# Kernel tuning notes

Hardware: AMD Instinct MI355X
Metric: run time of the kernel (lower is better)

## Reference

```python
import jax, jax.numpy as jnp
import numpy as np
from jax.scipy.special import logsumexp

S, D, K, R, P = 500, 768, 16, 256, 64  # seq_len, bert_dim, out_dim, n_pairs, max wordpieces/entity


def setup_inputs() -> dict:
    key = jax.random.key(0)
    k1, k2, k3, k4, k5, k6 = jax.random.split(key, 6)
    word_embeddings = jax.random.normal(k1, (S, D), jnp.float32)
    # kaiming_normal_ fan_in = D*K (last two dims collapsed); gain sqrt(2) for relu
    W = jax.random.normal(k2, (D, K, D), jnp.float32) * np.float32((2.0 / (K * D)) ** 0.5)
    idx1 = jax.random.randint(k3, (R, P), 0, S)
    idx2 = jax.random.randint(k4, (R, P), 0, S)
    # ragged mention lengths -> padding masks (at least 1 valid wordpiece)
    len1 = jax.random.randint(k5, (R,), 1, P + 1)
    len2 = jax.random.randint(k6, (R,), 1, P + 1)
    pos = jnp.arange(P)
    mask1 = (pos[None, :] < len1[:, None]).astype(jnp.float32)
    mask2 = (pos[None, :] < len2[:, None]).astype(jnp.float32)
    return {"word_embeddings": word_embeddings, "W": W, "idx1": idx1, "idx2": idx2,
            "mask1": mask1, "mask2": mask2}


def reference(word_embeddings, W, idx1, idx2, mask1, mask2):
    # gather ragged mention wordpieces (padded to P per entity)
    e1 = word_embeddings[idx1]  # [R, P, D]
    e2 = word_embeddings[idx2]  # [R, P, D]
    # biaffine: z[r,k,p,q] = e1[r,p,:] @ W[:,k,:] @ e2[r,q,:]
    zh = jnp.einsum('rpd,dke->rpke', e1, W)      # [R, P, K, D]
    z = jnp.einsum('rpke,rqe->rkpq', zh, e2)     # [R, K, P, P]
    # logsumexp pooling over all valid (p, q) mention-token pairs
    b = mask1[:, None, :, None] * mask2[:, None, None, :]  # [R, 1, P, P]
    scores = logsumexp(z, axis=(2, 3), b=b)      # [R, K]
    return scores
```

## Files before the change

### kernel.cpp

```cpp
#include <hip/hip_runtime.h>
#include <math.h>

#define S_ 500
#define D_ 768
#define K_ 16
#define R_ 256
#define P_ 64
#define NT 12

typedef unsigned short ushort_t;
typedef __attribute__((ext_vector_type(8))) short short8;
typedef __attribute__((ext_vector_type(4))) float floatx4;

__device__ inline ushort_t f2bf(float x) {
  unsigned int u = __float_as_uint(x);
  u += 0x7fffu + ((u >> 16) & 1u);
  return (ushort_t)(u >> 16);
}

#define GLD_LDS16(g, l)                                                        \
  __builtin_amdgcn_global_load_lds(                                            \
      (const __attribute__((address_space(1))) void*)(g),                      \
      (__attribute__((address_space(3))) void*)(l), 16, 0, 0)

#define ASM_BARRIER asm volatile("s_barrier" ::: "memory")
#define WAIT_VM8 asm volatile("s_waitcnt vmcnt(8)" ::: "memory")
#define WAIT_VM6 asm volatile("s_waitcnt vmcnt(6)" ::: "memory")
#define WAIT_VM0 asm volatile("s_waitcnt vmcnt(0)" ::: "memory")

__global__ __launch_bounds__(256) void prep(const float* __restrict__ WE,
                                            const float* __restrict__ W,
                                            ushort_t* __restrict__ WEb,
                                            ushort_t* __restrict__ Wt) {
  const int t = threadIdx.x;
  if (blockIdx.x < 384) {
    int gid = blockIdx.x * 256 + t;
    int row = gid / 192;
    ushort4 o = {0, 0, 0, 0};
    if (row < S_) {
      float4 v = *(const float4*)(WE + (size_t)gid * 4);
      o.x = f2bf(v.x); o.y = f2bf(v.y); o.z = f2bf(v.z); o.w = f2bf(v.w);
    }
    *(ushort4*)(WEb + (size_t)gid * 4) = o;
    return;
  }
  __shared__ float tile[64][68];
  const int tb = blockIdx.x - 384;
  const int n0 = (tb % 192) * 64, d0 = (tb / 192) * 64;
  {
    const int r = t >> 2, cbase = (t & 3) * 16;
#pragma unroll
    for (int i = 0; i < 4; i++) {
      float4 v = *(const float4*)(W + (size_t)(d0 + r) * 12288 + n0 + cbase + i * 4);
      *(float4*)&tile[r][cbase + i * 4] = v;
    }
  }
  __syncthreads();
  {
    const int bc = t & 15;
    const int br4 = (t >> 4) * 4;
    float4 tv[4];
#pragma unroll
    for (int ii = 0; ii < 4; ii++)
      tv[ii] = *(const float4*)&tile[bc * 4 + ii][br4];
#pragma unroll
    for (int j = 0; j < 4; j++) {
      ushort4 o;
      o.x = f2bf(((const float*)&tv[0])[j]);
      o.y = f2bf(((const float*)&tv[1])[j]);
      o.z = f2bf(((const float*)&tv[2])[j]);
      o.w = f2bf(((const float*)&tv[3])[j]);
      *(ushort4*)(Wt + (size_t)(n0 + br4 + j) * 768 + d0 + bc * 4) = o;
    }
  }
}

__global__ __launch_bounds__(256, 2) void mm0_bt(const ushort_t* __restrict__ A,
                                                 const ushort_t* __restrict__ Bm,
                                                 ushort_t* __restrict__ C) {
  __shared__ ushort_t As[2][2][128 * 32];
  __shared__ ushort_t Bs[2][2][128 * 32];
  const int tid = threadIdx.x;
  const int wave = tid >> 6, lane = tid & 63;
  const int m0 = blockIdx.y * 128, n0 = blockIdx.x * 128;
  const int wm = (wave & 1) * 64, wn = (wave >> 1) * 64;
  const int col = lane & 15, quad = lane >> 4;

  floatx4 acc[4][4];
#pragma unroll
  for (int i = 0; i < 4; i++)
#pragma unroll
    for (int j = 0; j < 4; j++)
#pragma unroll
      for (int e = 0; e < 4; e++) acc[i][j][e] = 0.f;

  const int srow = wave * 32 + (lane >> 2);
  const int scol = (lane & 3) * 8;
  const ushort_t* ga0 = A + (size_t)(m0 + srow) * D_ + scol;
  const ushort_t* gb0 = Bm + (size_t)(n0 + srow) * D_ + scol;
  const int ldsbase = (wave * 32) * 32;

#define ISSUE_TILE0(t_, buf_)                                                  \
  do {                                                                         \
    const ushort_t* ga = ga0 + (t_)*64;                                        \
    const ushort_t* gb = gb0 + (t_)*64;                                        \
    GLD_LDS16(ga, &As[buf_][0][ldsbase]);                                      \
    GLD_LDS16(ga + 16 * D_, &As[buf_][0][ldsbase + 16 * 32]);                  \
    GLD_LDS16(ga + 32, &As[buf_][1][ldsbase]);                                 \
    GLD_LDS16(ga + 32 + 16 * D_, &As[buf_][1][ldsbase + 16 * 32]);             \
    GLD_LDS16(gb, &Bs[buf_][0][ldsbase]);                                      \
    GLD_LDS16(gb + 16 * D_, &Bs[buf_][0][ldsbase + 16 * 32]);                  \
    GLD_LDS16(gb + 32, &Bs[buf_][1][ldsbase]);                                 \
    GLD_LDS16(gb + 32 + 16 * D_, &Bs[buf_][1][ldsbase + 16 * 32]);             \
  } while (0)

  ISSUE_TILE0(0, 0);
  for (int t = 0; t < NT; ++t) {
    const int cur = t & 1;
    if (t + 1 < NT) {
      ISSUE_TILE0(t + 1, cur ^ 1);
      WAIT_VM8;
    } else {
      WAIT_VM0;
    }
    ASM_BARRIER;
#pragma unroll
    for (int s = 0; s < 2; ++s) {
      short8 a[4], b[4];
#pragma unroll
      for (int i = 0; i < 4; i++)
        a[i] = *(const short8*)&As[cur][s][(wm + i * 16 + col) * 32 + quad * 8];
#pragma unroll
      for (int j = 0; j < 4; j++)
        b[j] = *(const short8*)&Bs[cur][s][(wn + j * 16 + col) * 32 + quad * 8];
#pragma unroll
      for (int i = 0; i < 4; i++)
#pragma unroll
        for (int j = 0; j < 4; j++)
          acc[i][j] = __builtin_amdgcn_mfma_f32_16x16x32_bf16(b[j], a[i], acc[i][j], 0, 0, 0);
    }
    ASM_BARRIER;
  }
#undef ISSUE_TILE0

#pragma unroll
  for (int i = 0; i < 4; i++) {
    int m = m0 + wm + i * 16 + col;
#pragma unroll
    for (int j = 0; j < 4; j++) {
      int n = n0 + wn + j * 16 + quad * 4;
      ushort4 o;
      o.x = f2bf(acc[i][j][0]); o.y = f2bf(acc[i][j][1]);
      o.z = f2bf(acc[i][j][2]); o.w = f2bf(acc[i][j][3]);
      *(ushort4*)(C + (size_t)m * 12288 + n) = o;
    }
  }
}

__global__ __launch_bounds__(256, 2) void mm1_bt(const ushort_t* __restrict__ A,
                                                 const ushort_t* __restrict__ Bm,
                                                 ushort_t* __restrict__ G) {
  __shared__ ushort_t As[2][2][128 * 32];
  __shared__ ushort_t Bs[2][2][64 * 32];
  const int tid = threadIdx.x;
  const int wave = tid >> 6, lane = tid & 63;
  const int m0 = blockIdx.y * 128, n0 = blockIdx.x * 64;
  const int wm = (wave & 1) * 64, wn = (wave >> 1) * 32;
  const int col = lane & 15, quad = lane >> 4;

  floatx4 acc[4][2];
#pragma unroll
  for (int i = 0; i < 4; i++)
#pragma unroll
    for (int j = 0; j < 2; j++)
#pragma unroll
      for (int e = 0; e < 4; e++) acc[i][j][e] = 0.f;

  const int lrow = lane >> 2, scol = (lane & 3) * 8;
  const ushort_t* ga0 = A + (size_t)(m0 + wave * 32 + lrow) * D_ + scol;
  const ushort_t* gb0 = Bm + (size_t)(n0 + wave * 16 + lrow) * D_ + scol;
  const int aoff = (wave * 32) * 32;
  const int boff = (wave * 16) * 32;

#define ISSUE_TILE1(t_, buf_)                                                  \
  do {                                                                         \
    _Pragma("unroll") for (int s_ = 0; s_ < 2; s_++) {                         \
      const ushort_t* ga = ga0 + (t_)*64 + s_ * 32;                            \
      const ushort_t* gb = gb0 + (t_)*64 + s_ * 32;                            \
      GLD_LDS16(ga, &As[buf_][s_][aoff]);                                      \
      GLD_LDS16(ga + 16 * D_, &As[buf_][s_][aoff + 16 * 32]);                  \
      GLD_LDS16(gb, &Bs[buf_][s_][boff]);                                      \
    }                                                                          \
  } while (0)

  ISSUE_TILE1(0, 0);
  for (int t = 0; t < NT; ++t) {
    const int cur = t & 1;
    if (t + 1 < NT) {
      ISSUE_TILE1(t + 1, cur ^ 1);
      WAIT_VM6;
    } else {
      WAIT_VM0;
    }
    ASM_BARRIER;
#pragma unroll
    for (int s = 0; s < 2; ++s) {
      short8 a[4], b[2];
#pragma unroll
      for (int i = 0; i < 4; i++)
        a[i] = *(const short8*)&As[cur][s][(wm + i * 16 + col) * 32 + quad * 8];
#pragma unroll
      for (int j = 0; j < 2; j++)
        b[j] = *(const short8*)&Bs[cur][s][(wn + j * 16 + col) * 32 + quad * 8];
#pragma unroll
      for (int i = 0; i < 4; i++)
#pragma unroll
        for (int j = 0; j < 2; j++)
          acc[i][j] = __builtin_amdgcn_mfma_f32_16x16x32_bf16(a[i], b[j], acc[i][j], 0, 0, 0);
    }
    ASM_BARRIER;
  }
#undef ISSUE_TILE1

#pragma unroll
  for (int i = 0; i < 4; i++) {
    int s1 = (m0 + wm + i * 16) >> 4;
#pragma unroll
    for (int j = 0; j < 2; j++) {
      int s2 = n0 + wn + j * 16 + col;
      if (s1 < S_ && s2 < S_) {
        ushort4 o;
        o.x = f2bf(acc[i][j][0]); o.y = f2bf(acc[i][j][1]);
        o.z = f2bf(acc[i][j][2]); o.w = f2bf(acc[i][j][3]);
        *(ushort4*)(G + (((size_t)s1 * S_ + s2) << 4) + quad * 4) = o;
      }
    }
  }
}

__global__ __launch_bounds__(256) void lse_kernel(const ushort_t* __restrict__ G,
                                                  const int* __restrict__ idx1,
                                                  const int* __restrict__ idx2,
                                                  const float* __restrict__ mask1,
                                                  const float* __restrict__ mask2,
                                                  float* __restrict__ out) {
  const int r = blockIdx.x;
  const int tid = threadIdx.x;
  __shared__ int b1[P_], b2[P_];
  __shared__ int s_len1, s_len2;
  __shared__ float wmx[4][K_], wsum[4][K_];

  if (tid < 64) {
    float mv = mask1[r * P_ + tid];
    unsigned long long bal = __ballot(mv > 0.5f);
    if (tid == 0) s_len1 = (int)__popcll(bal);
    b1[tid] = idx1[r * P_ + tid] * (S_ * K_);
  } else if (tid < 128) {
    int q = tid - 64;
    float mv = mask2[r * P_ + q];
    unsigned long long bal = __ballot(mv > 0.5f);
    if (q == 0) s_len2 = (int)__popcll(bal);
    b2[q] = idx2[r * P_ + q] * K_;
  }
  __syncthreads();
  const int len2 = s_len2;
  const int total = s_len1 * len2;

  float m[K_], s[K_];
#pragma unroll
  for (int k = 0; k < K_; k++) { m[k] = -3.0e38f; s[k] = 0.f; }

  for (int i = tid; i < total; i += 256) {
    int p = i / len2;
    int q = i - p * len2;
    const uint4* g4 = (const uint4*)(G + b1[p] + b2[q]);
    uint4 w0 = g4[0], w1 = g4[1];
    unsigned int uu[8] = {w0.x, w0.y, w0.z, w0.w, w1.x, w1.y, w1.z, w1.w};
    float z[K_];
#pragma unroll
    for (int h = 0; h < 8; h++) {
      z[2 * h + 0] = __uint_as_float(uu[h] << 16);
      z[2 * h + 1] = __uint_as_float(uu[h] & 0xffff0000u);
    }
#pragma unroll
    for (int k = 0; k < K_; k++) {
      float zk = z[k];
      float M2 = fmaxf(m[k], zk);
      s[k] = s[k] * __expf(m[k] - M2) + __expf(zk - M2);
      m[k] = M2;
    }
  }

#pragma unroll
  for (int off = 1; off < 64; off <<= 1) {
#pragma unroll
    for (int k = 0; k < K_; k++) {
      float mo = __shfl_xor(m[k], off, 64);
      float so = __shfl_xor(s[k], off, 64);
      float M2 = fmaxf(m[k], mo);
      s[k] = s[k] * __expf(m[k] - M2) + so * __expf(mo - M2);
      m[k] = M2;
    }
  }
  const int wave = tid >> 6, lane = tid & 63;
  if (lane == 0) {
#pragma unroll
    for (int k = 0; k < K_; k++) { wmx[wave][k] = m[k]; wsum[wave][k] = s[k]; }
  }
  __syncthreads();
  if (tid < K_) {
    float M = -3.0e38f, Ssum = 0.f;
#pragma unroll
    for (int w = 0; w < 4; w++) {
      float mo = wmx[w][tid], so = wsum[w][tid];
      float M2 = fmaxf(M, mo);
      Ssum = Ssum * __expf(M - M2) + so * __expf(mo - M2);
      M = M2;
    }
    out[r * K_ + tid] = M + __logf(Ssum);
  }
}

extern "C" void kernel_launch(void* const* d_in, const int* in_sizes, int n_in,
                              void* d_out, int out_size, void* d_ws, size_t ws_size,
                              hipStream_t stream) {
  const float* WE    = (const float*)d_in[0];
  const float* W     = (const float*)d_in[1];
  const int*   idx1  = (const int*)d_in[2];
  const int*   idx2  = (const int*)d_in[3];
  const float* mask1 = (const float*)d_in[4];
  const float* mask2 = (const float*)d_in[5];
  float* out = (float*)d_out;

  ushort_t* WEb   = (ushort_t*)d_ws;
  ushort_t* Wt    = WEb + (size_t)512 * 768;
  ushort_t* projb = Wt + (size_t)12288 * 768;
  ushort_t* G     = projb + (size_t)8192 * 768;

  prep<<<384 + 2304, 256, 0, stream>>>(WE, W, WEb, Wt);
  mm0_bt<<<dim3(96, 4), 256, 0, stream>>>(WEb, Wt, projb);
  mm1_bt<<<dim3(8, 64), 256, 0, stream>>>(projb, WEb, G);
  lse_kernel<<<R_, 256, 0, stream>>>(G, idx1, idx2, mask1, mask2, out);
}
```

Before: 143.6 us.

## Fuse prep, both GEMMs and logsumexp into one persistent kernel with atomic flags

Replaces four separate kernel launches with one persistent kernel of 512 blocks that run the phases in sequence. Global atomic counters act as inter-block barriers, and the second GEMM waits only on the first-GEMM row block it depends on. This removes launch gaps and the tail idle time between stages, so later stages can start early. The cost is a memset launch, spin-waiting, and a risk of deadlock if not all 512 blocks can be resident at once.

```diff
diff --git a/kernel.cpp b/kernel.cpp
--- a/kernel.cpp
+++ b/kernel.cpp
@@ -7,6 +7,7 @@
 #define R_ 256
 #define P_ 64
 #define NT 12
+#define NBLK 512
 
 typedef unsigned short ushort_t;
 typedef __attribute__((ext_vector_type(8))) short short8;
@@ -28,77 +29,101 @@
 #define WAIT_VM6 asm volatile("s_waitcnt vmcnt(6)" ::: "memory")
 #define WAIT_VM0 asm volatile("s_waitcnt vmcnt(0)" ::: "memory")
 
-__global__ __launch_bounds__(256) void prep(const float* __restrict__ WE,
-                                            const float* __restrict__ W,
-                                            ushort_t* __restrict__ WEb,
-                                            ushort_t* __restrict__ Wt) {
-  const int t = threadIdx.x;
-  if (blockIdx.x < 384) {
-    int gid = blockIdx.x * 256 + t;
-    int row = gid / 192;
-    ushort4 o = {0, 0, 0, 0};
-    if (row < S_) {
-      float4 v = *(const float4*)(WE + (size_t)gid * 4);
-      o.x = f2bf(v.x); o.y = f2bf(v.y); o.z = f2bf(v.z); o.w = f2bf(v.w);
-    }
-    *(ushort4*)(WEb + (size_t)gid * 4) = o;
-    return;
-  }
-  __shared__ float tile[64][68];
-  const int tb = blockIdx.x - 384;
-  const int n0 = (tb % 192) * 64, d0 = (tb / 192) * 64;
-  {
-    const int r = t >> 2, cbase = (t & 3) * 16;
-#pragma unroll
-    for (int i = 0; i < 4; i++) {
-      float4 v = *(const float4*)(W + (size_t)(d0 + r) * 12288 + n0 + cbase + i * 4);
-      *(float4*)&tile[r][cbase + i * 4] = v;
-    }
-  }
+__device__ __forceinline__ void phase_arrive(int* f) {
   __syncthreads();
-  {
-    const int bc = t & 15;
-    const int br4 = (t >> 4) * 4;
-    float4 tv[4];
-#pragma unroll
-    for (int ii = 0; ii < 4; ii++)
-      tv[ii] = *(const float4*)&tile[bc * 4 + ii][br4];
-#pragma unroll
-    for (int j = 0; j < 4; j++) {
-      ushort4 o;
-      o.x = f2bf(((const float*)&tv[0])[j]);
-      o.y = f2bf(((const float*)&tv[1])[j]);
-      o.z = f2bf(((const float*)&tv[2])[j]);
-      o.w = f2bf(((const float*)&tv[3])[j]);
-      *(ushort4*)(Wt + (size_t)(n0 + br4 + j) * 768 + d0 + bc * 4) = o;
-    }
-  }
-}
-
-__global__ __launch_bounds__(256, 2) void mm0_bt(const ushort_t* __restrict__ A,
-                                                 const ushort_t* __restrict__ Bm,
-                                                 ushort_t* __restrict__ C) {
-  __shared__ ushort_t As[2][2][128 * 32];
-  __shared__ ushort_t Bs[2][2][128 * 32];
+  __threadfence();
+  if (threadIdx.x == 0) atomicAdd(f, 1);
+}
+__device__ __forceinline__ void phase_wait(int* f, int target) {
+  if (threadIdx.x == 0) {
+    while (__hip_atomic_load(f, __ATOMIC_RELAXED, __HIP_MEMORY_SCOPE_AGENT) < target)
+      __builtin_amdgcn_s_sleep(2);
+  }
+  __syncthreads();
+  __threadfence();
+}
+
+__global__ __launch_bounds__(256, 2) void fused(
+    const float* __restrict__ WE, const float* __restrict__ W,
+    const int* __restrict__ idx1, const int* __restrict__ idx2,
+    const float* __restrict__ mask1, const float* __restrict__ mask2,
+    ushort_t* __restrict__ WEb, ushort_t* __restrict__ Wt,
+    ushort_t* __restrict__ projb, ushort_t* __restrict__ G,
+    int* __restrict__ flags, float* __restrict__ out) {
+  __shared__ __align__(16) char smem[65536];
+  const int bid = blockIdx.x;
   const int tid = threadIdx.x;
   const int wave = tid >> 6, lane = tid & 63;
-  const int m0 = blockIdx.y * 128, n0 = blockIdx.x * 128;
-  const int wm = (wave & 1) * 64, wn = (wave >> 1) * 64;
   const int col = lane & 15, quad = lane >> 4;
 
-  floatx4 acc[4][4];
-#pragma unroll
-  for (int i = 0; i < 4; i++)
-#pragma unroll
-    for (int j = 0; j < 4; j++)
-#pragma unroll
-      for (int e = 0; e < 4; e++) acc[i][j][e] = 0.f;
-
-  const int srow = wave * 32 + (lane >> 2);
-  const int scol = (lane & 3) * 8;
-  const ushort_t* ga0 = A + (size_t)(m0 + srow) * D_ + scol;
-  const ushort_t* gb0 = Bm + (size_t)(n0 + srow) * D_ + scol;
-  const int ldsbase = (wave * 32) * 32;
+  {
+    float(*tile)[68] = (float(*)[68])smem;
+    for (int u = bid; u < 2688; u += NBLK) {
+      if (u < 384) {
+        int gid = u * 256 + tid;
+        int row = gid / 192;
+        ushort4 o = {0, 0, 0, 0};
+        if (row < S_) {
+          float4 v = *(const float4*)(WE + (size_t)gid * 4);
+          o.x = f2bf(v.x); o.y = f2bf(v.y); o.z = f2bf(v.z); o.w = f2bf(v.w);
+        }
+        *(ushort4*)(WEb + (size_t)gid * 4) = o;
+      } else {
+        int tb = u - 384;
+        int n0 = (tb % 192) * 64, d0 = (tb / 192) * 64;
+        __syncthreads();
+        {
+          const int r = tid >> 2, cbase = (tid & 3) * 16;
+#pragma unroll
+          for (int i = 0; i < 4; i++) {
+            float4 v = *(const float4*)(W + (size_t)(d0 + r) * 12288 + n0 + cbase + i * 4);
+            *(float4*)&tile[r][cbase + i * 4] = v;
+          }
+        }
+        __syncthreads();
+        {
+          const int bc = tid & 15, br4 = (tid >> 4) * 4;
+          float4 tv[4];
+#pragma unroll
+          for (int ii = 0; ii < 4; ii++)
+            tv[ii] = *(const float4*)&tile[bc * 4 + ii][br4];
+#pragma unroll
+          for (int j = 0; j < 4; j++) {
+            ushort4 o;
+            o.x = f2bf(((const float*)&tv[0])[j]);
+            o.y = f2bf(((const float*)&tv[1])[j]);
+            o.z = f2bf(((const float*)&tv[2])[j]);
+            o.w = f2bf(((const float*)&tv[3])[j]);
+            *(ushort4*)(Wt + (size_t)(n0 + br4 + j) * 768 + d0 + bc * 4) = o;
+          }
+        }
+      }
+    }
+  }
+  phase_arrive(&flags[0]);
+  phase_wait(&flags[0], NBLK);
+
+  if (bid < 384) {
+    typedef ushort_t buf128[2][2][128 * 32];
+    buf128& As = *(buf128*)smem;
+    buf128& Bs = *(buf128*)(smem + 32768);
+    const int bx = bid % 96, by = bid / 96;
+    const int m0 = by * 128, n0 = bx * 128;
+    const int wm = (wave & 1) * 64, wn = (wave >> 1) * 64;
+
+    floatx4 acc[4][4];
+#pragma unroll
+    for (int i = 0; i < 4; i++)
+#pragma unroll
+      for (int j = 0; j < 4; j++)
+#pragma unroll
+        for (int e = 0; e < 4; e++) acc[i][j][e] = 0.f;
+
+    const int srow = wave * 32 + (lane >> 2);
+    const int scol = (lane & 3) * 8;
+    const ushort_t* ga0 = WEb + (size_t)(m0 + srow) * D_ + scol;
+    const ushort_t* gb0 = Wt + (size_t)(n0 + srow) * D_ + scol;
+    const int ldsbase = (wave * 32) * 32;
 
 #define ISSUE_TILE0(t_, buf_)                                                  \
   do {                                                                         \
@@ -114,73 +139,74 @@
     GLD_LDS16(gb + 32 + 16 * D_, &Bs[buf_][1][ldsbase + 16 * 32]);             \
   } while (0)
 
-  ISSUE_TILE0(0, 0);
-  for (int t = 0; t < NT; ++t) {
-    const int cur = t & 1;
-    if (t + 1 < NT) {
-      ISSUE_TILE0(t + 1, cur ^ 1);
-      WAIT_VM8;
-    } else {
-      WAIT_VM0;
-    }
-    ASM_BARRIER;
-#pragma unroll
-    for (int s = 0; s < 2; ++s) {
-      short8 a[4], b[4];
-#pragma unroll
-      for (int i = 0; i < 4; i++)
-        a[i] = *(const short8*)&As[cur][s][(wm + i * 16 + col) * 32 + quad * 8];
-#pragma unroll
-      for (int j = 0; j < 4; j++)
-        b[j] = *(const short8*)&Bs[cur][s][(wn + j * 16 + col) * 32 + quad * 8];
-#pragma unroll
-      for (int i = 0; i < 4; i++)
+    ISSUE_TILE0(0, 0);
+    for (int t = 0; t < NT; ++t) {
+      const int cur = t & 1;
+      if (t + 1 < NT) {
+        ISSUE_TILE0(t + 1, cur ^ 1);
+        WAIT_VM8;
+      } else {
+        WAIT_VM0;
+      }
+      ASM_BARRIER;
+#pragma unroll
+      for (int s = 0; s < 2; ++s) {
+        short8 a[4], b[4];
+#pragma unroll
+        for (int i = 0; i < 4; i++)
+          a[i] = *(const short8*)&As[cur][s][(wm + i * 16 + col) * 32 + quad * 8];
 #pragma unroll
         for (int j = 0; j < 4; j++)
-          acc[i][j] = __builtin_amdgcn_mfma_f32_16x16x32_bf16(b[j], a[i], acc[i][j], 0, 0, 0);
-    }
-    ASM_BARRIER;
-  }
+          b[j] = *(const short8*)&Bs[cur][s][(wn + j * 16 + col) * 32 + quad * 8];
+#pragma unroll
+        for (int i = 0; i < 4; i++)
+#pragma unroll
+          for (int j = 0; j < 4; j++)
+            acc[i][j] = __builtin_amdgcn_mfma_f32_16x16x32_bf16(b[j], a[i], acc[i][j], 0, 0, 0);
+      }
+      ASM_BARRIER;
+    }
 #undef ISSUE_TILE0
 
 #pragma unroll
-  for (int i = 0; i < 4; i++) {
-    int m = m0 + wm + i * 16 + col;
-#pragma unroll
-    for (int j = 0; j < 4; j++) {
-      int n = n0 + wn + j * 16 + quad * 4;
-      ushort4 o;
-      o.x = f2bf(acc[i][j][0]); o.y = f2bf(acc[i][j][1]);
-      o.z = f2bf(acc[i][j][2]); o.w = f2bf(acc[i][j][3]);
-      *(ushort4*)(C + (size_t)m * 12288 + n) = o;
-    }
-  }
-}
-
-__global__ __launch_bounds__(256, 2) void mm1_bt(const ushort_t* __restrict__ A,
-                                                 const ushort_t* __restrict__ Bm,
-                                                 ushort_t* __restrict__ G) {
-  __shared__ ushort_t As[2][2][128 * 32];
-  __shared__ ushort_t Bs[2][2][64 * 32];
-  const int tid = threadIdx.x;
-  const int wave = tid >> 6, lane = tid & 63;
-  const int m0 = blockIdx.y * 128, n0 = blockIdx.x * 64;
-  const int wm = (wave & 1) * 64, wn = (wave >> 1) * 32;
-  const int col = lane & 15, quad = lane >> 4;
-
-  floatx4 acc[4][2];
-#pragma unroll
-  for (int i = 0; i < 4; i++)
-#pragma unroll
-    for (int j = 0; j < 2; j++)
-#pragma unroll
-      for (int e = 0; e < 4; e++) acc[i][j][e] = 0.f;
-
-  const int lrow = lane >> 2, scol = (lane & 3) * 8;
-  const ushort_t* ga0 = A + (size_t)(m0 + wave * 32 + lrow) * D_ + scol;
-  const ushort_t* gb0 = Bm + (size_t)(n0 + wave * 16 + lrow) * D_ + scol;
-  const int aoff = (wave * 32) * 32;
-  const int boff = (wave * 16) * 32;
+    for (int i = 0; i < 4; i++) {
+      int m = m0 + wm + i * 16 + col;
+#pragma unroll
+      for (int j = 0; j < 4; j++) {
+        int n = n0 + wn + j * 16 + quad * 4;
+        ushort4 o;
+        o.x = f2bf(acc[i][j][0]); o.y = f2bf(acc[i][j][1]);
+        o.z = f2bf(acc[i][j][2]); o.w = f2bf(acc[i][j][3]);
+        *(ushort4*)(projb + (size_t)m * 12288 + n) = o;
+      }
+    }
+    phase_arrive(&flags[1 + by]);
+  }
+
+  {
+    typedef ushort_t abuf[2][2][128 * 32];
+    typedef ushort_t bbuf[2][2][64 * 32];
+    abuf& As = *(abuf*)smem;
+    bbuf& Bs = *(bbuf*)(smem + 32768);
+    const int mby = bid >> 3, mbx = bid & 7;
+    const int m0 = mby * 128, n0 = mbx * 64;
+    const int wm = (wave & 1) * 64, wn = (wave >> 1) * 32;
+
+    phase_wait(&flags[1 + (mby >> 4)], 96);
+
+    floatx4 acc[4][2];
+#pragma unroll
+    for (int i = 0; i < 4; i++)
+#pragma unroll
+      for (int j = 0; j < 2; j++)
+#pragma unroll
+        for (int e = 0; e < 4; e++) acc[i][j][e] = 0.f;
+
+    const int lrow = lane >> 2, scol = (lane & 3) * 8;
+    const ushort_t* ga0 = projb + (size_t)(m0 + wave * 32 + lrow) * D_ + scol;
+    const ushort_t* gb0 = WEb + (size_t)(n0 + wave * 16 + lrow) * D_ + scol;
+    const int aoff = (wave * 32) * 32;
+    const int boff = (wave * 16) * 32;
 
 #define ISSUE_TILE1(t_, buf_)                                                  \
   do {                                                                         \
@@ -193,131 +219,130 @@
     }                                                                          \
   } while (0)
 
-  ISSUE_TILE1(0, 0);
-  for (int t = 0; t < NT; ++t) {
-    const int cur = t & 1;
-    if (t + 1 < NT) {
-      ISSUE_TILE1(t + 1, cur ^ 1);
-      WAIT_VM6;
-    } else {
-      WAIT_VM0;
-    }
-    ASM_BARRIER;
-#pragma unroll
-    for (int s = 0; s < 2; ++s) {
-      short8 a[4], b[2];
-#pragma unroll
-      for (int i = 0; i < 4; i++)
-        a[i] = *(const short8*)&As[cur][s][(wm + i * 16 + col) * 32 + quad * 8];
-#pragma unroll
-      for (int j = 0; j < 2; j++)
-        b[j] = *(const short8*)&Bs[cur][s][(wn + j * 16 + col) * 32 + quad * 8];
-#pragma unroll
-      for (int i = 0; i < 4; i++)
+    ISSUE_TILE1(0, 0);
+    for (int t = 0; t < NT; ++t) {
+      const int cur = t & 1;
+      if (t + 1 < NT) {
+        ISSUE_TILE1(t + 1, cur ^ 1);
+        WAIT_VM6;
+      } else {
+        WAIT_VM0;
+      }
+      ASM_BARRIER;
+#pragma unroll
+      for (int s = 0; s < 2; ++s) {
+        short8 a[4], b[2];
+#pragma unroll
+        for (int i = 0; i < 4; i++)
+          a[i] = *(const short8*)&As[cur][s][(wm + i * 16 + col) * 32 + quad * 8];
 #pragma unroll
         for (int j = 0; j < 2; j++)
-          acc[i][j] = __builtin_amdgcn_mfma_f32_16x16x32_bf16(a[i], b[j], acc[i][j], 0, 0, 0);
-    }
-    ASM_BARRIER;
-  }
+          b[j] = *(const short8*)&Bs[cur][s][(wn + j * 16 + col) * 32 + quad * 8];
+#pragma unroll
+        for (int i = 0; i < 4; i++)
+#pragma unroll
+          for (int j = 0; j < 2; j++)
+            acc[i][j] = __builtin_amdgcn_mfma_f32_16x16x32_bf16(a[i], b[j], acc[i][j], 0, 0, 0);
+      }
+      ASM_BARRIER;
+    }
 #undef ISSUE_TILE1
 
 #pragma unroll
-  for (int i = 0; i < 4; i++) {
-    int s1 = (m0 + wm + i * 16) >> 4;
-#pragma unroll
-    for (int j = 0; j < 2; j++) {
-      int s2 = n0 + wn + j * 16 + col;
-      if (s1 < S_ && s2 < S_) {
-        ushort4 o;
-        o.x = f2bf(acc[i][j][0]); o.y = f2bf(acc[i][j][1]);
-        o.z = f2bf(acc[i][j][2]); o.w = f2bf(acc[i][j][3]);
-        *(ushort4*)(G + (((size_t)s1 * S_ + s2) << 4) + quad * 4) = o;
-      }
-    }
-  }
-}
-
-__global__ __launch_bounds__(256) void lse_kernel(const ushort_t* __restrict__ G,
-                                                  const int* __restrict__ idx1,
-                                                  const int* __restrict__ idx2,
-                                                  const float* __restrict__ mask1,
-                                                  const float* __restrict__ mask2,
-                                                  float* __restrict__ out) {
-  const int r = blockIdx.x;
-  const int tid = threadIdx.x;
-  __shared__ int b1[P_], b2[P_];
-  __shared__ int s_len1, s_len2;
-  __shared__ float wmx[4][K_], wsum[4][K_];
-
-  if (tid < 64) {
-    float mv = mask1[r * P_ + tid];
-    unsigned long long bal = __ballot(mv > 0.5f);
-    if (tid == 0) s_len1 = (int)__popcll(bal);
-    b1[tid] = idx1[r * P_ + tid] * (S_ * K_);
-  } else if (tid < 128) {
-    int q = tid - 64;
-    float mv = mask2[r * P_ + q];
-    unsigned long long bal = __ballot(mv > 0.5f);
-    if (q == 0) s_len2 = (int)__popcll(bal);
-    b2[q] = idx2[r * P_ + q] * K_;
-  }
-  __syncthreads();
-  const int len2 = s_len2;
-  const int total = s_len1 * len2;
-
-  float m[K_], s[K_];
-#pragma unroll
-  for (int k = 0; k < K_; k++) { m[k] = -3.0e38f; s[k] = 0.f; }
-
-  for (int i = tid; i < total; i += 256) {
-    int p = i / len2;
-    int q = i - p * len2;
-    const uint4* g4 = (const uint4*)(G + b1[p] + b2[q]);
-    uint4 w0 = g4[0], w1 = g4[1];
-    unsigned int uu[8] = {w0.x, w0.y, w0.z, w0.w, w1.x, w1.y, w1.z, w1.w};
-    float z[K_];
-#pragma unroll
-    for (int h = 0; h < 8; h++) {
-      z[2 * h + 0] = __uint_as_float(uu[h] << 16);
-      z[2 * h + 1] = __uint_as_float(uu[h] & 0xffff0000u);
-    }
-#pragma unroll
-    for (int k = 0; k < K_; k++) {
-      float zk = z[k];
-      float M2 = fmaxf(m[k], zk);
-      s[k] = s[k] * __expf(m[k] - M2) + __expf(zk - M2);
-      m[k] = M2;
-    }
-  }
-
-#pragma unroll
-  for (int off = 1; off < 64; off <<= 1) {
-#pragma unroll
-    for (int k = 0; k < K_; k++) {
-      float mo = __shfl_xor(m[k], off, 64);
-      float so = __shfl_xor(s[k], off, 64);
-      float M2 = fmaxf(m[k], mo);
-      s[k] = s[k] * __expf(m[k] - M2) + so * __expf(mo - M2);
-      m[k] = M2;
-    }
-  }
-  const int wave = tid >> 6, lane = tid & 63;
-  if (lane == 0) {
-#pragma unroll
-    for (int k = 0; k < K_; k++) { wmx[wave][k] = m[k]; wsum[wave][k] = s[k]; }
-  }
-  __syncthreads();
-  if (tid < K_) {
-    float M = -3.0e38f, Ssum = 0.f;
-#pragma unroll
-    for (int w = 0; w < 4; w++) {
-      float mo = wmx[w][tid], so = wsum[w][tid];
-      float M2 = fmaxf(M, mo);
-      Ssum = Ssum * __expf(M - M2) + so * __expf(mo - M2);
-      M = M2;
-    }
-    out[r * K_ + tid] = M + __logf(Ssum);
+    for (int i = 0; i < 4; i++) {
+      int s1 = (m0 + wm + i * 16) >> 4;
+#pragma unroll
+      for (int j = 0; j < 2; j++) {
+        int s2 = n0 + wn + j * 16 + col;
+        if (s1 < S_ && s2 < S_) {
+          ushort4 o;
+          o.x = f2bf(acc[i][j][0]); o.y = f2bf(acc[i][j][1]);
+          o.z = f2bf(acc[i][j][2]); o.w = f2bf(acc[i][j][3]);
+          *(ushort4*)(G + (((size_t)s1 * S_ + s2) << 4) + quad * 4) = o;
+        }
+      }
+    }
+  }
+  phase_arrive(&flags[5]);
+
+  if (bid >= 256) return;
+  phase_wait(&flags[5], NBLK);
+  {
+    int* b1 = (int*)smem;
+    int* b2 = b1 + P_;
+    float* wmx = (float*)(b2 + P_);
+    float* wsum = wmx + 4 * K_;
+    int* slen = (int*)(wsum + 4 * K_);
+    const int r = bid;
+
+    if (tid < 64) {
+      float mv = mask1[r * P_ + tid];
+      unsigned long long bal = __ballot(mv > 0.5f);
+      if (tid == 0) slen[0] = (int)__popcll(bal);
+      b1[tid] = idx1[r * P_ + tid] * (S_ * K_);
+    } else if (tid < 128) {
+      int q = tid - 64;
+      float mv = mask2[r * P_ + q];
+      unsigned long long bal = __ballot(mv > 0.5f);
+      if (q == 0) slen[1] = (int)__popcll(bal);
+      b2[q] = idx2[r * P_ + q] * K_;
+    }
+    __syncthreads();
+    const int len2 = slen[1];
+    const int total = slen[0] * len2;
+
+    float m[K_], s[K_];
+#pragma unroll
+    for (int k = 0; k < K_; k++) { m[k] = -3.0e38f; s[k] = 0.f; }
+
+    for (int i = tid; i < total; i += 256) {
+      int p = i / len2;
+      int q = i - p * len2;
+      const uint4* g4 = (const uint4*)(G + b1[p] + b2[q]);
+      uint4 w0 = g4[0], w1 = g4[1];
+      unsigned int uu[8] = {w0.x, w0.y, w0.z, w0.w, w1.x, w1.y, w1.z, w1.w};
+      float z[K_];
+#pragma unroll
+      for (int h = 0; h < 8; h++) {
+        z[2 * h + 0] = __uint_as_float(uu[h] << 16);
+        z[2 * h + 1] = __uint_as_float(uu[h] & 0xffff0000u);
+      }
+#pragma unroll
+      for (int k = 0; k < K_; k++) {
+        float zk = z[k];
+        float M2 = fmaxf(m[k], zk);
+        s[k] = s[k] * __expf(m[k] - M2) + __expf(zk - M2);
+        m[k] = M2;
+      }
+    }
+
+#pragma unroll
+    for (int off = 1; off < 64; off <<= 1) {
+#pragma unroll
+      for (int k = 0; k < K_; k++) {
+        float mo = __shfl_xor(m[k], off, 64);
+        float so = __shfl_xor(s[k], off, 64);
+        float M2 = fmaxf(m[k], mo);
+        s[k] = s[k] * __expf(m[k] - M2) + so * __expf(mo - M2);
+        m[k] = M2;
+      }
+    }
+    if (lane == 0) {
+#pragma unroll
+      for (int k = 0; k < K_; k++) { wmx[wave * K_ + k] = m[k]; wsum[wave * K_ + k] = s[k]; }
+    }
+    __syncthreads();
+    if (tid < K_) {
+      float M = -3.0e38f, Ssum = 0.f;
+#pragma unroll
+      for (int w = 0; w < 4; w++) {
+        float mo = wmx[w * K_ + tid], so = wsum[w * K_ + tid];
+        float M2 = fmaxf(M, mo);
+        Ssum = Ssum * __expf(M - M2) + so * __expf(mo - M2);
+        M = M2;
+      }
+      out[r * K_ + tid] = M + __logf(Ssum);
+    }
   }
 }
 
@@ -332,13 +357,13 @@
   const float* mask2 = (const float*)d_in[5];
   float* out = (float*)d_out;
 
-  ushort_t* WEb   = (ushort_t*)d_ws;
+  int*      flags = (int*)d_ws;
+  ushort_t* WEb   = (ushort_t*)((char*)d_ws + 256);
   ushort_t* Wt    = WEb + (size_t)512 * 768;
   ushort_t* projb = Wt + (size_t)12288 * 768;
   ushort_t* G     = projb + (size_t)8192 * 768;
 
-  prep<<<384 + 2304, 256, 0, stream>>>(WE, W, WEb, Wt);
-  mm0_bt<<<dim3(96, 4), 256, 0, stream>>>(WEb, Wt, projb);
-  mm1_bt<<<dim3(8, 64), 256, 0, stream>>>(projb, WEb, G);
-  lse_kernel<<<R_, 256, 0, stream>>>(G, idx1, idx2, mask1, mask2, out);
-}
+  hipMemsetAsync(flags, 0, 64, stream);
+  fused<<<NBLK, 256, 0, stream>>>(WE, W, idx1, idx2, mask1, mask2,
+                                  WEb, Wt, projb, G, flags, out);
+}
```

Result: slower. 446.2 us (+210.8%).
